# Kernel optimization log

Measured on AMD Instinct MI355X. Metric: run time of the kernel, lower is better.

Reference implementation:

```python
import jax, jax.numpy as jnp
import numpy as np

B, L, D = 4, 4096, 256
INIT_ALPHA = -2.0
INV_TEMP = 1.0 / 0.1


def setup_inputs() -> dict:
    key = jax.random.key(0)
    k1, k2, k3, k4 = jax.random.split(key, 4)
    latents = jax.random.normal(k1, (B, L, D), dtype=jnp.float32)
    current_coords = jax.random.normal(k2, (B, L, 2), dtype=jnp.float32)
    # Linear(D, D, bias=False) weights (torch stores [out, in]; y = x @ W.T)
    lim = 1.0 / np.sqrt(D)
    Wq = jax.random.uniform(k3, (D, D), minval=-lim, maxval=lim, dtype=jnp.float32)
    Wk = jax.random.uniform(k4, (D, D), minval=-lim, maxval=lim, dtype=jnp.float32)
    alpha_raw = jnp.asarray(INIT_ALPHA, dtype=jnp.float32)
    return {"latents": latents, "current_coords": current_coords,
            "Wq": Wq, "Wk": Wk, "alpha_raw": alpha_raw, "layer_idx": 3}


def _l2norm(x, eps=1e-12):
    # F.normalize(dim=-1): x / max(||x||, eps)
    n = jnp.sqrt(jnp.sum(x * x, axis=-1, keepdims=True))
    return x / jnp.maximum(n, eps)


def reference(latents, current_coords, Wq, Wk, alpha_raw, layer_idx):
    # pred_idx selection (share_weights=True): 0 if layer_idx==0 else 1;
    # layer_idx=3 -> params given are for pred_idx=1.
    q = _l2norm(jnp.einsum('bld,ed->ble', latents, Wq))  # [B,L,D]
    k = _l2norm(jnp.einsum('bld,ed->ble', latents, Wk))  # [B,L,D]
    scores = jnp.einsum('bld,bmd->blm', q, k) * INV_TEMP  # [B,L,L]
    scores = jnp.clip(scores, -50.0, 50.0)
    W = jax.nn.softmax(scores, axis=-1)                   # [B,L,L]
    alpha = jax.nn.sigmoid(alpha_raw)
    # M = alpha*W + (1-alpha)*I; M @ coords == alpha*(W@coords) + (1-alpha)*coords
    new_coords = alpha * jnp.einsum('blm,bmc->blc', W, current_coords) \
                 + (1.0 - alpha) * current_coords
    displacement = new_coords - current_coords
    return (new_coords, displacement)
```

## Files before the change

kernel.cpp:

```cpp
#include <hip/hip_runtime.h>
#include <hip/hip_bf16.h>

#define BB 4
#define LL 4096
#define DD 256
#define MM (BB * LL)
#define NSPLIT 8
#define BM 256
#define NQB (LL / BM)
#define KPS (LL / NSPLIT)
#define KT 64
#define NKT (KPS / KT)

typedef short short8 __attribute__((ext_vector_type(8)));
typedef float floatx4 __attribute__((ext_vector_type(4)));

#define SCALE_LOG2E 14.426950408889634f

__device__ __forceinline__ unsigned short f2bf(float f) {
    __hip_bfloat16 h = __float2bfloat16(f);
    union { __hip_bfloat16 h; unsigned short s; } c; c.h = h; return c.s;
}

__device__ __forceinline__ float fast_exp2(float x) {
#if __has_builtin(__builtin_amdgcn_exp2f)
    return __builtin_amdgcn_exp2f(x);
#else
    return exp2f(x);
#endif
}

__device__ __forceinline__ void stage16(const char* g, char* l, int lane) {
#if __has_builtin(__builtin_amdgcn_global_load_lds)
    __builtin_amdgcn_global_load_lds(
        (const __attribute__((address_space(1))) void*)(g + lane * 16),
        (__attribute__((address_space(3))) void*)l, 16, 0, 0);
#else
    *(short8*)(l + lane * 16) = *(const short8*)(g + lane * 16);
#endif
}

__global__ __launch_bounds__(256) void cvt_swz_kernel(
    const float* __restrict__ srcq, const float* __restrict__ srck,
    unsigned short* __restrict__ dstq, unsigned short* __restrict__ dstk)
{
    const int which = blockIdx.x >> 5;
    const float* src = which ? srck : srcq;
    unsigned short* dst = which ? dstk : dstq;
    const int t = (blockIdx.x & 31) * 256 + threadIdx.x;
    const int r = t >> 5, c = t & 31;
    const float4 v0 = ((const float4*)src)[t * 2];
    const float4 v1 = ((const float4*)src)[t * 2 + 1];
    short8 o;
    o[0] = (short)f2bf(v0.x); o[1] = (short)f2bf(v0.y);
    o[2] = (short)f2bf(v0.z); o[3] = (short)f2bf(v0.w);
    o[4] = (short)f2bf(v1.x); o[5] = (short)f2bf(v1.y);
    o[6] = (short)f2bf(v1.z); o[7] = (short)f2bf(v1.w);
    const int cs = c ^ (r & 7);
    *(short8*)(dst + (size_t)r * DD + cs * 8) = o;
}

__global__ __launch_bounds__(256) void proj_norm_kernel(
    const float* __restrict__ latents,
    const __hip_bfloat16* __restrict__ Wq,
    const __hip_bfloat16* __restrict__ Wk,
    __hip_bfloat16* __restrict__ qn,
    __hip_bfloat16* __restrict__ kn)
{
    __shared__ char lds[65536];

    const int tid  = threadIdx.x;
    const int wave = tid >> 6;
    const int lane = tid & 63;
    const int n15  = lane & 15;
    const int quad = lane >> 4;
    const int sw   = n15 & 7;

    const int pass  = blockIdx.x & 1;
    const int rbase = (blockIdx.x >> 1) * 64;
    const int m0    = rbase + wave * 16;
    const int r160  = rbase >> 4;

    short8 afrag[8];
    const float* Abase = latents + (size_t)(m0 + n15) * DD + quad * 8;
#pragma unroll
    for (int kk = 0; kk < 8; ++kk) {
        const float4 v0 = *(const float4*)(Abase + kk * 32);
        const float4 v1 = *(const float4*)(Abase + kk * 32 + 4);
        short8 f;
        f[0] = (short)f2bf(v0.x); f[1] = (short)f2bf(v0.y);
        f[2] = (short)f2bf(v0.z); f[3] = (short)f2bf(v0.w);
        f[4] = (short)f2bf(v1.x); f[5] = (short)f2bf(v1.y);
        f[6] = (short)f2bf(v1.z); f[7] = (short)f2bf(v1.w);
        afrag[kk] = f;
    }

    const char* W = (const char*)(pass ? Wk : Wq);

    floatx4 acc[16];
#pragma unroll
    for (int ct = 0; ct < 16; ++ct) acc[ct] = (floatx4){0.f, 0.f, 0.f, 0.f};

    {
        const char* src = W + wave * 8192;
        char* dst = lds + wave * 8192;
#pragma unroll
        for (int j = 0; j < 8; ++j) stage16(src + j * 1024, dst + j * 1024, lane);
    }

    for (int round = 0; round < 4; ++round) {
        __syncthreads();
        if (round + 1 < 4) {
            const char* src = W + (size_t)(round + 1) * 32768 + wave * 8192;
            char* dst = lds + ((round + 1) & 1) * 32768 + wave * 8192;
#pragma unroll
            for (int j = 0; j < 8; ++j) stage16(src + j * 1024, dst + j * 1024, lane);
        }
        const char* buf = lds + (round & 1) * 32768;
#pragma unroll
        for (int jt = 0; jt < 4; ++jt) {
            const int ct = round * 4 + jt;
            const char* lbase = buf + (jt * 16 + n15) * 512;
            floatx4 a = acc[ct];
#pragma unroll
            for (int kk = 0; kk < 8; ++kk) {
                const int chunk = (4 * kk + quad) ^ sw;
                short8 bfr = *(const short8*)(lbase + chunk * 16);
                a = __builtin_amdgcn_mfma_f32_16x16x32_bf16(afrag[kk], bfr, a, 0, 0, 0);
            }
            acc[ct] = a;
        }
    }

    float ss[4] = {0.f, 0.f, 0.f, 0.f};
#pragma unroll
    for (int ct = 0; ct < 16; ++ct)
#pragma unroll
        for (int r = 0; r < 4; ++r) ss[r] += acc[ct][r] * acc[ct][r];
#pragma unroll
    for (int r = 0; r < 4; ++r) {
        ss[r] += __shfl_xor(ss[r], 1, 64);
        ss[r] += __shfl_xor(ss[r], 2, 64);
        ss[r] += __shfl_xor(ss[r], 4, 64);
        ss[r] += __shfl_xor(ss[r], 8, 64);
    }
    float sc[4];
#pragma unroll
    for (int r = 0; r < 4; ++r) {
        sc[r] = 1.f / fmaxf(sqrtf(ss[r]), 1e-12f);
        if (pass == 0) sc[r] *= SCALE_LOG2E;
    }

    unsigned short* tb = (unsigned short*)lds;
#pragma unroll
    for (int h = 0; h < 2; ++h) {
        __syncthreads();
#pragma unroll
        for (int cth = 0; cth < 8; ++cth) {
            const int ct = h * 8 + cth;
            const int col = cth * 16 + n15;
#pragma unroll
            for (int r = 0; r < 4; ++r) {
                const int rl = wave * 16 + quad * 4 + r;
                tb[rl * 136 + col] = f2bf(acc[ct][r] * sc[r]);
            }
        }
        __syncthreads();
        if (pass == 0) {
#pragma unroll
            for (int j = 0; j < 4; ++j) {
                const int g = tid + j * 256;
                const int n15r = g & 15, q2 = (g >> 4) & 3, kkh = (g >> 6) & 3, r16l = (g >> 8) & 3;
                const int rl = r16l * 16 + n15r;
                short8 v = *(const short8*)(tb + rl * 136 + kkh * 32 + q2 * 8);
                const size_t chunk = (((size_t)(r160 + r16l) * 8 + (h * 4 + kkh)) * 4 + q2) * 16 + n15r;
                *(short8*)((char*)qn + chunk * 16) = v;
            }
        } else {
#pragma unroll
            for (int j = 0; j < 4; ++j) {
                const int g = tid + j * 256;
                const int csl = g & 15, rl = g >> 4;
                const int row = rbase + rl;
                const int ci = csl ^ (row & 7);
                short8 v = *(const short8*)(tb + rl * 136 + ci * 8);
                *(short8*)((char*)kn + (size_t)row * 512 + (h * 16 + csl) * 16) = v;
            }
        }
    }
}

__global__ __launch_bounds__(512) void attn_kernel(
    const __hip_bfloat16* __restrict__ qn,
    const __hip_bfloat16* __restrict__ kn,
    const float* __restrict__ coords,
    float* __restrict__ partials)
{
    __shared__ char lds[2 * 32768];

    const int tid  = threadIdx.x;
    const int wave = tid >> 6;
    const int lane = tid & 63;
    const int n15  = lane & 15;
    const int quad = lane >> 4;
    const int sw   = n15 & 7;

    int bs = blockIdx.x;
    const int qb    = bs % NQB;    bs /= NQB;
    const int split = bs % NSPLIT; bs /= NSPLIT;
    const int b     = bs;

    const int mw = b * LL + qb * BM + wave * 32;

    const int key_base = b * LL + split * KPS;
    const char* ksrc = (const char*)kn + (size_t)key_base * 512;

    {
        const char* src = ksrc + wave * 4096;
        char* dst = lds + wave * 4096;
#pragma unroll
        for (int j = 0; j < 4; ++j) stage16(src + j * 1024, dst + j * 1024, lane);
    }

    short8 aq[2][8];
    const int t16 = mw >> 4;
#pragma unroll
    for (int rt = 0; rt < 2; ++rt)
#pragma unroll
        for (int kk = 0; kk < 8; ++kk) {
            const size_t chunk = (((size_t)(t16 + rt) * 8 + kk) * 4 + quad) * 16 + n15;
            aq[rt][kk] = *(const short8*)((const char*)qn + chunk * 16);
        }

    float s0[2][4], s1[2][4], s2[2][4];
#pragma unroll
    for (int rt = 0; rt < 2; ++rt)
#pragma unroll
        for (int r = 0; r < 4; ++r) { s0[rt][r] = 0.f; s1[rt][r] = 0.f; s2[rt][r] = 0.f; }

    for (int kt = 0; kt < NKT; ++kt) {
        __syncthreads();
        if (kt + 1 < NKT) {
            const char* src = ksrc + (size_t)(kt + 1) * KT * 512 + wave * 4096;
            char* dst = lds + ((kt + 1) & 1) * 32768 + wave * 4096;
#pragma unroll
            for (int j = 0; j < 4; ++j) stage16(src + j * 1024, dst + j * 1024, lane);
        }
        const char* buf = lds + (kt & 1) * 32768;

#pragma unroll
        for (int ct = 0; ct < 4; ++ct) {
            const int kidx = key_base + kt * KT + ct * 16 + n15;
            const float2 cc = *(const float2*)(coords + (size_t)kidx * 2);

            floatx4 acc0 = (floatx4){0.f, 0.f, 0.f, 0.f};
            floatx4 acc1 = (floatx4){0.f, 0.f, 0.f, 0.f};
            const char* lbase = buf + (ct * 16 + n15) * 512;
#pragma unroll
            for (int kk = 0; kk < 8; ++kk) {
                const int chunk = (4 * kk + quad) ^ sw;
                short8 bfr = *(const short8*)(lbase + chunk * 16);
                acc0 = __builtin_amdgcn_mfma_f32_16x16x32_bf16(aq[0][kk], bfr, acc0, 0, 0, 0);
                acc1 = __builtin_amdgcn_mfma_f32_16x16x32_bf16(aq[1][kk], bfr, acc1, 0, 0, 0);
            }
#pragma unroll
            for (int r = 0; r < 4; ++r) {
                const float e0 = fast_exp2(acc0[r]);
                const float e1 = fast_exp2(acc1[r]);
                s0[0][r] += e0;
                s1[0][r] = fmaf(cc.x, e0, s1[0][r]);
                s2[0][r] = fmaf(cc.y, e0, s2[0][r]);
                s0[1][r] += e1;
                s1[1][r] = fmaf(cc.x, e1, s1[1][r]);
                s2[1][r] = fmaf(cc.y, e1, s2[1][r]);
            }
        }
    }

#pragma unroll
    for (int rt = 0; rt < 2; ++rt)
#pragma unroll
        for (int r = 0; r < 4; ++r)
#pragma unroll
            for (int mask = 1; mask <= 8; mask <<= 1) {
                s0[rt][r] += __shfl_xor(s0[rt][r], mask, 64);
                s1[rt][r] += __shfl_xor(s1[rt][r], mask, 64);
                s2[rt][r] += __shfl_xor(s2[rt][r], mask, 64);
            }

    if (n15 == 0) {
#pragma unroll
        for (int rt = 0; rt < 2; ++rt)
#pragma unroll
            for (int r = 0; r < 4; ++r) {
                const int m = mw + rt * 16 + quad * 4 + r;
                float* p = partials + ((size_t)split * MM + m) * 4;
                p[0] = s0[rt][r];
                p[1] = s1[rt][r];
                p[2] = s2[rt][r];
            }
    }
}

__global__ __launch_bounds__(256) void finish_kernel(
    const float* __restrict__ partials,
    const float* __restrict__ coords,
    const float* __restrict__ alpha_raw,
    float* __restrict__ out)
{
    const int m = blockIdx.x * 256 + threadIdx.x;

    const float alpha = 1.f / (1.f + __expf(-alpha_raw[0]));

    float s0 = 0.f, s1 = 0.f, s2 = 0.f;
#pragma unroll
    for (int s = 0; s < NSPLIT; ++s) {
        const float4 v = *(const float4*)(partials + ((size_t)s * MM + m) * 4);
        s0 += v.x; s1 += v.y; s2 += v.z;
    }

    const float cx = coords[m * 2];
    const float cy = coords[m * 2 + 1];
    const float inv = 1.f / s0;
    const float nx = alpha * (s1 * inv) + (1.f - alpha) * cx;
    const float ny = alpha * (s2 * inv) + (1.f - alpha) * cy;

    out[m * 2]     = nx;
    out[m * 2 + 1] = ny;
    out[2 * MM + m * 2]     = nx - cx;
    out[2 * MM + m * 2 + 1] = ny - cy;
}

extern "C" void kernel_launch(void* const* d_in, const int* in_sizes, int n_in,
                              void* d_out, int out_size, void* d_ws, size_t ws_size,
                              hipStream_t stream) {
    const float* latents   = (const float*)d_in[0];
    const float* coords    = (const float*)d_in[1];
    const float* Wq        = (const float*)d_in[2];
    const float* Wk        = (const float*)d_in[3];
    const float* alpha_raw = (const float*)d_in[4];

    char* ws = (char*)d_ws;
    __hip_bfloat16* qn   = (__hip_bfloat16*)ws;
    __hip_bfloat16* kn   = (__hip_bfloat16*)(ws + (size_t)8 * 1024 * 1024);
    __hip_bfloat16* wq_b = (__hip_bfloat16*)(ws + (size_t)16 * 1024 * 1024);
    __hip_bfloat16* wk_b = (__hip_bfloat16*)(ws + (size_t)16 * 1024 * 1024 + 131072);
    float* partials      = (float*)(ws + (size_t)16 * 1024 * 1024 + 262144);

    float* out = (float*)d_out;

    cvt_swz_kernel<<<64, 256, 0, stream>>>(Wq, Wk, (unsigned short*)wq_b, (unsigned short*)wk_b);
    proj_norm_kernel<<<512, 256, 0, stream>>>(latents, wq_b, wk_b, qn, kn);
    attn_kernel<<<BB * NQB * NSPLIT, 512, 0, stream>>>(qn, kn, coords, partials);
    finish_kernel<<<MM / 256, 256, 0, stream>>>(partials, coords, alpha_raw, out);
}
```

Baseline: 121.5 us.

## Use 4 waves with 64 query rows each and remap block order

The attention kernel drops to 256 threads per block, and each wave now handles 64 query rows (4 row tiles) instead of 32, so every K fragment read from LDS feeds four MFMAs. Each wave stages twice as much of the K tile. The block index is permuted so that consecutive blocks spread across splits and batches. This cuts LDS read traffic per FLOP, at the cost of more registers per thread and fewer waves per block for hiding latency.

```diff
diff --git a/kernel.cpp b/kernel.cpp
--- a/kernel.cpp
+++ b/kernel.cpp
@@ -190,7 +190,7 @@
     }
 }
 
-__global__ __launch_bounds__(512) void attn_kernel(
+__global__ __launch_bounds__(256, 2) void attn_kernel(
     const __hip_bfloat16* __restrict__ qn,
     const __hip_bfloat16* __restrict__ kn,
     const float* __restrict__ coords,
@@ -205,46 +205,46 @@
     const int quad = lane >> 4;
     const int sw   = n15 & 7;
 
-    int bs = blockIdx.x;
+    int bs = (blockIdx.x & 7) * 64 + (blockIdx.x >> 3);
     const int qb    = bs % NQB;    bs /= NQB;
     const int split = bs % NSPLIT; bs /= NSPLIT;
     const int b     = bs;
 
-    const int mw = b * LL + qb * BM + wave * 32;
+    const int mw = b * LL + qb * BM + wave * 64;
 
     const int key_base = b * LL + split * KPS;
     const char* ksrc = (const char*)kn + (size_t)key_base * 512;
 
     {
-        const char* src = ksrc + wave * 4096;
-        char* dst = lds + wave * 4096;
-#pragma unroll
-        for (int j = 0; j < 4; ++j) stage16(src + j * 1024, dst + j * 1024, lane);
-    }
-
-    short8 aq[2][8];
+        const char* src = ksrc + wave * 8192;
+        char* dst = lds + wave * 8192;
+#pragma unroll
+        for (int j = 0; j < 8; ++j) stage16(src + j * 1024, dst + j * 1024, lane);
+    }
+
+    short8 aq[4][8];
     const int t16 = mw >> 4;
 #pragma unroll
-    for (int rt = 0; rt < 2; ++rt)
+    for (int rt = 0; rt < 4; ++rt)
 #pragma unroll
         for (int kk = 0; kk < 8; ++kk) {
             const size_t chunk = (((size_t)(t16 + rt) * 8 + kk) * 4 + quad) * 16 + n15;
             aq[rt][kk] = *(const short8*)((const char*)qn + chunk * 16);
         }
 
-    float s0[2][4], s1[2][4], s2[2][4];
-#pragma unroll
-    for (int rt = 0; rt < 2; ++rt)
+    float s0[4][4], s1[4][4], s2[4][4];
+#pragma unroll
+    for (int rt = 0; rt < 4; ++rt)
 #pragma unroll
         for (int r = 0; r < 4; ++r) { s0[rt][r] = 0.f; s1[rt][r] = 0.f; s2[rt][r] = 0.f; }
 
     for (int kt = 0; kt < NKT; ++kt) {
         __syncthreads();
         if (kt + 1 < NKT) {
-            const char* src = ksrc + (size_t)(kt + 1) * KT * 512 + wave * 4096;
-            char* dst = lds + ((kt + 1) & 1) * 32768 + wave * 4096;
-#pragma unroll
-            for (int j = 0; j < 4; ++j) stage16(src + j * 1024, dst + j * 1024, lane);
+            const char* src = ksrc + (size_t)(kt + 1) * KT * 512 + wave * 8192;
+            char* dst = lds + ((kt + 1) & 1) * 32768 + wave * 8192;
+#pragma unroll
+            for (int j = 0; j < 8; ++j) stage16(src + j * 1024, dst + j * 1024, lane);
         }
         const char* buf = lds + (kt & 1) * 32768;
 
@@ -253,32 +253,32 @@
             const int kidx = key_base + kt * KT + ct * 16 + n15;
             const float2 cc = *(const float2*)(coords + (size_t)kidx * 2);
 
-            floatx4 acc0 = (floatx4){0.f, 0.f, 0.f, 0.f};
-            floatx4 acc1 = (floatx4){0.f, 0.f, 0.f, 0.f};
+            floatx4 acc[4];
+#pragma unroll
+            for (int rt = 0; rt < 4; ++rt) acc[rt] = (floatx4){0.f, 0.f, 0.f, 0.f};
             const char* lbase = buf + (ct * 16 + n15) * 512;
 #pragma unroll
             for (int kk = 0; kk < 8; ++kk) {
                 const int chunk = (4 * kk + quad) ^ sw;
-                short8 bfr = *(const short8*)(lbase + chunk * 16);
-                acc0 = __builtin_amdgcn_mfma_f32_16x16x32_bf16(aq[0][kk], bfr, acc0, 0, 0, 0);
-                acc1 = __builtin_amdgcn_mfma_f32_16x16x32_bf16(aq[1][kk], bfr, acc1, 0, 0, 0);
-            }
-#pragma unroll
-            for (int r = 0; r < 4; ++r) {
-                const float e0 = fast_exp2(acc0[r]);
-                const float e1 = fast_exp2(acc1[r]);
-                s0[0][r] += e0;
-                s1[0][r] = fmaf(cc.x, e0, s1[0][r]);
-                s2[0][r] = fmaf(cc.y, e0, s2[0][r]);
-                s0[1][r] += e1;
-                s1[1][r] = fmaf(cc.x, e1, s1[1][r]);
-                s2[1][r] = fmaf(cc.y, e1, s2[1][r]);
-            }
-        }
-    }
-
-#pragma unroll
-    for (int rt = 0; rt < 2; ++rt)
+                const short8 bfr = *(const short8*)(lbase + chunk * 16);
+#pragma unroll
+                for (int rt = 0; rt < 4; ++rt)
+                    acc[rt] = __builtin_amdgcn_mfma_f32_16x16x32_bf16(aq[rt][kk], bfr, acc[rt], 0, 0, 0);
+            }
+#pragma unroll
+            for (int rt = 0; rt < 4; ++rt)
+#pragma unroll
+                for (int r = 0; r < 4; ++r) {
+                    const float e = fast_exp2(acc[rt][r]);
+                    s0[rt][r] += e;
+                    s1[rt][r] = fmaf(cc.x, e, s1[rt][r]);
+                    s2[rt][r] = fmaf(cc.y, e, s2[rt][r]);
+                }
+        }
+    }
+
+#pragma unroll
+    for (int rt = 0; rt < 4; ++rt)
 #pragma unroll
         for (int r = 0; r < 4; ++r)
 #pragma unroll
@@ -290,7 +290,7 @@
 
     if (n15 == 0) {
 #pragma unroll
-        for (int rt = 0; rt < 2; ++rt)
+        for (int rt = 0; rt < 4; ++rt)
 #pragma unroll
             for (int r = 0; r < 4; ++r) {
                 const int m = mw + rt * 16 + quad * 4 + r;
@@ -351,6 +351,6 @@
 
     cvt_swz_kernel<<<64, 256, 0, stream>>>(Wq, Wk, (unsigned short*)wq_b, (unsigned short*)wk_b);
     proj_norm_kernel<<<512, 256, 0, stream>>>(latents, wq_b, wk_b, qn, kn);
-    attn_kernel<<<BB * NQB * NSPLIT, 512, 0, stream>>>(qn, kn, coords, partials);
+    attn_kernel<<<BB * NQB * NSPLIT, 256, 0, stream>>>(qn, kn, coords, partials);
     finish_kernel<<<MM / 256, 256, 0, stream>>>(partials, coords, alpha_raw, out);
 }
```

After: 126.4 us. +4.1%, slower.

## Store K and weights in MFMA fragment order; remap block indices for L2 locality

Applied to the files above, without the earlier changes.

Converts the bf16 weights and the normalized K to the same fragment-major layout already used for Q. Each lane then reads contiguous 16-byte chunks from LDS, with no XOR swizzle, in both the projection and attention MFMA loops. It also remaps block indices so blocks sharing a weight matrix or key split are scheduled together, and raises wave priority around the projection MFMA loop. The aim is lower LDS address arithmetic, fewer bank conflicts and better L2 reuse, at the cost of a layout that must stay consistent across three kernels.

```diff
diff --git a/kernel.cpp b/kernel.cpp
--- a/kernel.cpp
+++ b/kernel.cpp
@@ -17,6 +17,7 @@
 
 #define SCALE_LOG2E 14.426950408889634f
 
+
 __device__ __forceinline__ unsigned short f2bf(float f) {
     __hip_bfloat16 h = __float2bfloat16(f);
     union { __hip_bfloat16 h; unsigned short s; } c; c.h = h; return c.s;
@@ -40,7 +41,7 @@
 #endif
 }
 
-__global__ __launch_bounds__(256) void cvt_swz_kernel(
+__global__ __launch_bounds__(256) void cvt_fm_kernel(
     const float* __restrict__ srcq, const float* __restrict__ srck,
     unsigned short* __restrict__ dstq, unsigned short* __restrict__ dstk)
 {
@@ -56,8 +57,8 @@
     o[2] = (short)f2bf(v0.z); o[3] = (short)f2bf(v0.w);
     o[4] = (short)f2bf(v1.x); o[5] = (short)f2bf(v1.y);
     o[6] = (short)f2bf(v1.z); o[7] = (short)f2bf(v1.w);
-    const int cs = c ^ (r & 7);
-    *(short8*)(dst + (size_t)r * DD + cs * 8) = o;
+    const int chunk = (r >> 4) * 512 + c * 16 + (r & 15);
+    *(short8*)(dst + (size_t)chunk * 8) = o;
 }
 
 __global__ __launch_bounds__(256) void proj_norm_kernel(
@@ -74,10 +75,10 @@
     const int lane = tid & 63;
     const int n15  = lane & 15;
     const int quad = lane >> 4;
-    const int sw   = n15 & 7;
-
-    const int pass  = blockIdx.x & 1;
-    const int rbase = (blockIdx.x >> 1) * 64;
+
+    const int pass  = (blockIdx.x >> 3) & 1;
+    const int pidx  = (blockIdx.x & 7) | ((blockIdx.x >> 4) << 3);
+    const int rbase = pidx * 64;
     const int m0    = rbase + wave * 16;
     const int r160  = rbase >> 4;
 
@@ -120,14 +121,15 @@
 #pragma unroll
         for (int jt = 0; jt < 4; ++jt) {
             const int ct = round * 4 + jt;
-            const char* lbase = buf + (jt * 16 + n15) * 512;
+            const char* lbase = buf + jt * 8192 + lane * 16;
             floatx4 a = acc[ct];
+            __builtin_amdgcn_s_setprio(1);
 #pragma unroll
             for (int kk = 0; kk < 8; ++kk) {
-                const int chunk = (4 * kk + quad) ^ sw;
-                short8 bfr = *(const short8*)(lbase + chunk * 16);
+                short8 bfr = *(const short8*)(lbase + kk * 1024);
                 a = __builtin_amdgcn_mfma_f32_16x16x32_bf16(afrag[kk], bfr, a, 0, 0, 0);
             }
+            __builtin_amdgcn_s_setprio(0);
             acc[ct] = a;
         }
     }
@@ -151,6 +153,7 @@
         if (pass == 0) sc[r] *= SCALE_LOG2E;
     }
 
+    __hip_bfloat16* dstp = pass ? kn : qn;
     unsigned short* tb = (unsigned short*)lds;
 #pragma unroll
     for (int h = 0; h < 2; ++h) {
@@ -166,26 +169,14 @@
             }
         }
         __syncthreads();
-        if (pass == 0) {
-#pragma unroll
-            for (int j = 0; j < 4; ++j) {
-                const int g = tid + j * 256;
-                const int n15r = g & 15, q2 = (g >> 4) & 3, kkh = (g >> 6) & 3, r16l = (g >> 8) & 3;
-                const int rl = r16l * 16 + n15r;
-                short8 v = *(const short8*)(tb + rl * 136 + kkh * 32 + q2 * 8);
-                const size_t chunk = (((size_t)(r160 + r16l) * 8 + (h * 4 + kkh)) * 4 + q2) * 16 + n15r;
-                *(short8*)((char*)qn + chunk * 16) = v;
-            }
-        } else {
-#pragma unroll
-            for (int j = 0; j < 4; ++j) {
-                const int g = tid + j * 256;
-                const int csl = g & 15, rl = g >> 4;
-                const int row = rbase + rl;
-                const int ci = csl ^ (row & 7);
-                short8 v = *(const short8*)(tb + rl * 136 + ci * 8);
-                *(short8*)((char*)kn + (size_t)row * 512 + (h * 16 + csl) * 16) = v;
-            }
+#pragma unroll
+        for (int j = 0; j < 4; ++j) {
+            const int g = tid + j * 256;
+            const int n15r = g & 15, q2 = (g >> 4) & 3, kkh = (g >> 6) & 3, r16l = (g >> 8) & 3;
+            const int rl = r16l * 16 + n15r;
+            short8 v = *(const short8*)(tb + rl * 136 + kkh * 32 + q2 * 8);
+            const size_t chunk = (((size_t)(r160 + r16l) * 8 + (h * 4 + kkh)) * 4 + q2) * 16 + n15r;
+            *(short8*)((char*)dstp + chunk * 16) = v;
         }
     }
 }
@@ -203,9 +194,8 @@
     const int lane = tid & 63;
     const int n15  = lane & 15;
     const int quad = lane >> 4;
-    const int sw   = n15 & 7;
-
-    int bs = blockIdx.x;
+
+    int bs = (blockIdx.x & 7) * 64 + (blockIdx.x >> 3);
     const int qb    = bs % NQB;    bs /= NQB;
     const int split = bs % NSPLIT; bs /= NSPLIT;
     const int b     = bs;
@@ -255,11 +245,10 @@
 
             floatx4 acc0 = (floatx4){0.f, 0.f, 0.f, 0.f};
             floatx4 acc1 = (floatx4){0.f, 0.f, 0.f, 0.f};
-            const char* lbase = buf + (ct * 16 + n15) * 512;
+            const char* lbase = buf + ct * 8192 + lane * 16;
 #pragma unroll
             for (int kk = 0; kk < 8; ++kk) {
-                const int chunk = (4 * kk + quad) ^ sw;
-                short8 bfr = *(const short8*)(lbase + chunk * 16);
+                short8 bfr = *(const short8*)(lbase + kk * 1024);
                 acc0 = __builtin_amdgcn_mfma_f32_16x16x32_bf16(aq[0][kk], bfr, acc0, 0, 0, 0);
                 acc1 = __builtin_amdgcn_mfma_f32_16x16x32_bf16(aq[1][kk], bfr, acc1, 0, 0, 0);
             }
@@ -349,7 +338,7 @@
 
     float* out = (float*)d_out;
 
-    cvt_swz_kernel<<<64, 256, 0, stream>>>(Wq, Wk, (unsigned short*)wq_b, (unsigned short*)wk_b);
+    cvt_fm_kernel<<<64, 256, 0, stream>>>(Wq, Wk, (unsigned short*)wq_b, (unsigned short*)wk_b);
     proj_norm_kernel<<<512, 256, 0, stream>>>(latents, wq_b, wk_b, qn, kn);
     attn_kernel<<<BB * NQB * NSPLIT, 512, 0, stream>>>(qn, kn, coords, partials);
     finish_kernel<<<MM / 256, 256, 0, stream>>>(partials, coords, alpha_raw, out);
```

Result: no change. 120.9 us (-0.5%).
